# Kernel tuning notes

Measured on AMD Instinct MI355X. Metric: run time of the kernel, lower is better.

The kernel has to match this reference:

```python
import jax, jax.numpy as jnp
import numpy as np

H = 8          # num heads
LN_EPS = 1e-5  # torch LayerNorm default

_SHAPES = {
    'src': (1024, 8, 256), 'pos': (1024, 8, 256), 'query_embed': (80, 8, 256), 'cam_mask': (8, 80, 1024),
    'enc_qkv_w': (2, 768, 256), 'enc_qkv_b': (2, 768), 'enc_out_w': (2, 256, 256), 'enc_out_b': (2, 256),
    'enc_ln1_g': (2, 256), 'enc_ln1_b': (2, 256),
    'enc_ff1_w': (2, 2048, 256), 'enc_ff1_b': (2, 2048), 'enc_ff2_w': (2, 256, 2048), 'enc_ff2_b': (2, 256),
    'enc_ln2_g': (2, 256), 'enc_ln2_b': (2, 256),
    'dec_sa_qkv_w': (2, 768, 256), 'dec_sa_qkv_b': (2, 768), 'dec_sa_out_w': (2, 256, 256), 'dec_sa_out_b': (2, 256),
    'dec_ln1_g': (2, 256), 'dec_ln1_b': (2, 256),
    'dec_ca_qkv_w': (2, 768, 256), 'dec_ca_qkv_b': (2, 768), 'dec_ca_out_w': (2, 256, 256), 'dec_ca_out_b': (2, 256),
    'dec_ln2_g': (2, 256), 'dec_ln2_b': (2, 256),
    'dec_ff1_w': (2, 2048, 256), 'dec_ff1_b': (2, 2048), 'dec_ff2_w': (2, 256, 2048), 'dec_ff2_b': (2, 256),
    'dec_ln3_g': (2, 256), 'dec_ln3_b': (2, 256),
    'dec_norm_g': (256,), 'dec_norm_b': (256,),
}


def setup_inputs() -> dict:
    key = jax.random.key(0)
    out = {}
    for i, (name, sh) in enumerate(_SHAPES.items()):
        k = jax.random.fold_in(key, i)
        if name.endswith('_g'):
            out[name] = jnp.ones(sh, jnp.float32)
        elif name.endswith('ln1_b') or name.endswith('ln2_b') or name.endswith('ln3_b') or name == 'dec_norm_b':
            out[name] = jnp.zeros(sh, jnp.float32)
        else:
            scale = 1.0 if name in ('src', 'pos', 'query_embed', 'cam_mask') else 0.02
            out[name] = jax.random.normal(k, sh, dtype=jnp.float32) * scale
    return out


def layer_norm(x, g, b):
    mu = jnp.mean(x, axis=-1, keepdims=True)
    var = jnp.mean(jnp.square(x - mu), axis=-1, keepdims=True)
    return (x - mu) * jax.lax.rsqrt(var + LN_EPS) * g + b


def mha(q_in, k_in, v_in, qkv_w, qkv_b, out_w, out_b, bias=None):
    # q_in: [L,B,D], k_in/v_in: [S,B,D]; torch layout: projections are x @ W.T + b
    L, B, D = q_in.shape
    S = k_in.shape[0]
    hd = D // H
    wq, wk, wv = qkv_w[:D], qkv_w[D:2 * D], qkv_w[2 * D:]
    bq, bk, bv = qkv_b[:D], qkv_b[D:2 * D], qkv_b[2 * D:]
    q = (q_in @ wq.T + bq).reshape(L, B, H, hd).transpose(1, 2, 0, 3)  # [B,H,L,hd]
    k = (k_in @ wk.T + bk).reshape(S, B, H, hd).transpose(1, 2, 0, 3)  # [B,H,S,hd]
    v = (v_in @ wv.T + bv).reshape(S, B, H, hd).transpose(1, 2, 0, 3)
    logits = jnp.einsum('bhld,bhsd->bhls', q, k) * (1.0 / np.sqrt(hd))
    if bias is not None:
        logits = logits + bias[:, None, :, :]  # CAM bias broadcast over heads
    attn = jax.nn.softmax(logits, axis=-1)
    o = jnp.einsum('bhls,bhsd->bhld', attn, v).transpose(2, 0, 1, 3).reshape(L, B, D)
    return o @ out_w.T + out_b


def reference(src, pos, query_embed, cam_mask,
              enc_qkv_w, enc_qkv_b, enc_out_w, enc_out_b, enc_ln1_g, enc_ln1_b,
              enc_ff1_w, enc_ff1_b, enc_ff2_w, enc_ff2_b, enc_ln2_g, enc_ln2_b,
              dec_sa_qkv_w, dec_sa_qkv_b, dec_sa_out_w, dec_sa_out_b, dec_ln1_g, dec_ln1_b,
              dec_ca_qkv_w, dec_ca_qkv_b, dec_ca_out_w, dec_ca_out_b, dec_ln2_g, dec_ln2_b,
              dec_ff1_w, dec_ff1_b, dec_ff2_w, dec_ff2_b, dec_ln3_g, dec_ln3_b,
              dec_norm_g, dec_norm_b):
    n_enc = enc_qkv_w.shape[0]
    n_dec = dec_sa_qkv_w.shape[0]
    # --- encoder (post-norm DETR style, pos added to q,k) ---
    mem = src
    for i in range(n_enc):
        qk = mem + pos
        a = mha(qk, qk, mem, enc_qkv_w[i], enc_qkv_b[i], enc_out_w[i], enc_out_b[i])
        mem = layer_norm(mem + a, enc_ln1_g[i], enc_ln1_b[i])
        f = jax.nn.relu(mem @ enc_ff1_w[i].T + enc_ff1_b[i]) @ enc_ff2_w[i].T + enc_ff2_b[i]
        mem = layer_norm(mem + f, enc_ln2_g[i], enc_ln2_b[i])
    # --- decoder: tgt starts at zeros (Q2L), query_embed is query_pos ---
    tgt = jnp.zeros_like(query_embed)
    for i in range(n_dec):
        qk = tgt + query_embed
        sa = mha(qk, qk, tgt, dec_sa_qkv_w[i], dec_sa_qkv_b[i], dec_sa_out_w[i], dec_sa_out_b[i])
        tgt = layer_norm(tgt + sa, dec_ln1_g[i], dec_ln1_b[i])
        ca = mha(tgt + query_embed, mem + pos, mem,
                 dec_ca_qkv_w[i], dec_ca_qkv_b[i], dec_ca_out_w[i], dec_ca_out_b[i],
                 bias=cam_mask)  # MA: CAM-derived additive attention bias [B,L,S]
        tgt = layer_norm(tgt + ca, dec_ln2_g[i], dec_ln2_b[i])
        f = jax.nn.relu(tgt @ dec_ff1_w[i].T + dec_ff1_b[i]) @ dec_ff2_w[i].T + dec_ff2_b[i]
        tgt = layer_norm(tgt + f, dec_ln3_g[i], dec_ln3_b[i])
    out = layer_norm(tgt, dec_norm_g, dec_norm_b)
    return out[None]  # [1, L, B, D] as in TransformerDecoder's output.unsqueeze(0)
```

## Files before the change

### kernel.cpp

```cpp
#include <hip/hip_runtime.h>
#include <hip/hip_bf16.h>
#include <cstdint>
#include <cstddef>

typedef __hip_bfloat16 bf16;
typedef float f4 __attribute__((ext_vector_type(4)));
typedef float f32x4 __attribute__((ext_vector_type(4)));
typedef short s8v __attribute__((ext_vector_type(8)));
typedef unsigned short u16x4 __attribute__((ext_vector_type(4)));
typedef unsigned short u16x8 __attribute__((ext_vector_type(8)));

#define LN_EPS 1e-5f
#define LOG2E 1.4426950408889634f

#if __has_builtin(__builtin_amdgcn_exp2f)
__device__ __forceinline__ float EXP2(float x) { return __builtin_amdgcn_exp2f(x); }
#else
__device__ __forceinline__ float EXP2(float x) {
  float r; asm("v_exp_f32 %0, %1" : "=v"(r) : "v"(x)); return r;
}
#endif

__device__ __forceinline__ void async_cp16(const void* g, void* lds) {
  __builtin_amdgcn_global_load_lds(
      (const __attribute__((address_space(1))) unsigned int*)g,
      (__attribute__((address_space(3))) unsigned int*)lds, 16, 0, 0);
}

__device__ __forceinline__ uint32_t pkbf(float lo, float hi) {
#if __has_builtin(__builtin_amdgcn_perm)
  uint32_t l = __builtin_bit_cast(uint32_t, lo) + 0x8000u;
  uint32_t h = __builtin_bit_cast(uint32_t, hi) + 0x8000u;
  return __builtin_amdgcn_perm(h, l, 0x07060302u);
#else
  uint32_t l = __builtin_bit_cast(uint32_t, lo) + 0x8000u;
  uint32_t h = __builtin_bit_cast(uint32_t, hi) + 0x8000u;
  return (l >> 16) | (h & 0xFFFF0000u);
#endif
}

#define NCAST 16
struct CastArgs {
  const float* in[NCAST];
  bf16* out[NCAST];
  int end4[NCAST];
  int nseg;
};

__global__ __launch_bounds__(256) void cast_multi(CastArgs a, int total4) {
  int i = blockIdx.x * 256 + threadIdx.x;
  if (i >= total4) return;
  int s = 0;
  while (i >= a.end4[s]) ++s;
  int j = i - (s ? a.end4[s - 1] : 0);
  f4 v = ((const f4*)a.in[s])[j];
  u16x4 o;
#pragma unroll
  for (int c = 0; c < 4; ++c) {
    bf16 h = __float2bfloat16(v[c]);
    o[c] = *reinterpret_cast<unsigned short*>(&h);
  }
  ((u16x4*)a.out[s])[j] = o;
}

__global__ __launch_bounds__(256) void scale_f32_kernel(const float* __restrict__ in,
                                                        float* __restrict__ out,
                                                        float s, int n4) {
  int i = blockIdx.x * 256 + threadIdx.x;
  if (i < n4) {
    f4 v = ((const f4*)in)[i];
    ((f4*)out)[i] = v * s;
  }
}

__global__ __launch_bounds__(256) void add_bf16_kernel(const float* __restrict__ a,
                                                       const float* __restrict__ b,
                                                       bf16* __restrict__ out, int n4) {
  int i = blockIdx.x * 256 + threadIdx.x;
  if (i < n4) {
    f4 x = ((const f4*)a)[i];
    f4 y = ((const f4*)b)[i];
    u16x4 o;
#pragma unroll
    for (int j = 0; j < 4; ++j) {
      bf16 h = __float2bfloat16(x[j] + y[j]);
      o[j] = *reinterpret_cast<unsigned short*>(&h);
    }
    ((u16x4*)out)[i] = o;
  }
}

template <int TB, int MODE, int SPLITK>
__global__ __launch_bounds__(256, 2) void mfma_gemm(
    const bf16* __restrict__ A, const bf16* __restrict__ W,
    const float* __restrict__ bias, float* __restrict__ C,
    bf16* __restrict__ Cb, int M, int N, int K, int HL, float qscale) {
  constexpr int WM = TB / 2, WN = TB / 2;
  constexpr int MR = WM / 16, NR = WN / 16;
  constexpr int NCH = TB / 32;
  __shared__ __attribute__((aligned(16))) unsigned short SH[TB * 128];
  unsigned short (*As)[64] = (unsigned short(*)[64])SH;
  unsigned short (*Ws)[64] = (unsigned short(*)[64])(SH + TB * 64);
  const int tid = threadIdx.x;
  const int lane = tid & 63, wave = tid >> 6;
  const int wr = wave >> 1, wc = wave & 1;
  const int bm = blockIdx.x * TB, bn = blockIdx.y * TB;
  const int fr = lane & 15, fo = lane >> 4;
  const int srowi = lane >> 3;
  const int slot = lane & 7;
  const int gcol = (slot ^ srowi) * 8;

  const int kchunk = K / SPLITK;
  const int kbeg = (SPLITK > 1) ? blockIdx.z * kchunk : 0;

  f32x4 acc[MR][NR] = {};

  for (int k0 = kbeg; k0 < kbeg + kchunk; k0 += 64) {
    __syncthreads();
#pragma unroll
    for (int c = 0; c < NCH; ++c) {
      int rbase = wave * (TB / 4) + c * 8;
      int row = rbase + srowi;
      async_cp16(A + (size_t)(bm + row) * K + k0 + gcol, &As[rbase][0]);
      async_cp16(W + (size_t)(bn + row) * K + k0 + gcol, &Ws[rbase][0]);
    }
    __syncthreads();
#pragma unroll
    for (int ks = 0; ks < 2; ++ks) {
      s8v a[MR], b[NR];
#pragma unroll
      for (int mi = 0; mi < MR; ++mi) {
        int row = wr * WM + mi * 16 + fr;
        a[mi] = *(const s8v*)((const char*)&As[0][0] + row * 128 +
                              ((ks * 64 + fo * 16) ^ ((row & 7) << 4)));
      }
#pragma unroll
      for (int ni = 0; ni < NR; ++ni) {
        int row = wc * WN + ni * 16 + fr;
        b[ni] = *(const s8v*)((const char*)&Ws[0][0] + row * 128 +
                              ((ks * 64 + fo * 16) ^ ((row & 7) << 4)));
      }
#pragma unroll
      for (int mi = 0; mi < MR; ++mi)
#pragma unroll
        for (int ni = 0; ni < NR; ++ni)
          acc[mi][ni] = __builtin_amdgcn_mfma_f32_16x16x32_bf16(
              a[mi], b[ni], acc[mi][ni], 0, 0, 0);
    }
  }

  const int r0 = (lane >> 4) * 4;

  if (MODE == 5) {
    __syncthreads();
    unsigned short (*T)[72] = (unsigned short(*)[72])SH;
#pragma unroll
    for (int mi = 0; mi < MR; ++mi)
#pragma unroll
      for (int ni = 0; ni < NR; ++ni) {
        int colL = wc * WN + ni * 16 + fr;
        float bv = bias[bn + colL];
#pragma unroll
        for (int r = 0; r < 4; ++r) {
          int rowL = wr * WM + mi * 16 + r0 + r;
          bf16 hv = __float2bfloat16(acc[mi][ni][r] + bv);
          T[colL][rowL] = *(unsigned short*)&hv;
        }
      }
    __syncthreads();
    const int lbase = bm >> 3;
#pragma unroll
    for (int jj = 0; jj < 2; ++jj) {
      int cid = tid * 2 + jj;
      int colL = cid >> 3, bb = cid & 7;
      int c = bn + colL;
      int sec = c >> 8, hh = (c >> 5) & 7, d = c & 31;
      u16x8 v;
#pragma unroll
      for (int l = 0; l < 8; ++l) v[l] = T[colL][bb + 8 * l];
      *(u16x8*)(Cb + (size_t)sec * ((size_t)64 * 32 * HL) +
                ((size_t)(bb * 8 + hh) * 32 + d) * HL + lbase) = v;
    }
    return;
  }

  float* Cz = (MODE == 4) ? C + (size_t)blockIdx.z * M * N : C;
#pragma unroll
  for (int mi = 0; mi < MR; ++mi) {
#pragma unroll
    for (int ni = 0; ni < NR; ++ni) {
      int col = bn + wc * WN + ni * 16 + fr;
      float bv = (MODE == 4) ? 0.f : bias[col];
#pragma unroll
      for (int r = 0; r < 4; ++r) {
        int row = bm + wr * WM + mi * 16 + r0 + r;
        float t = acc[mi][ni][r] + bv;
        if (MODE == 2) t = fmaxf(t, 0.f);
        if (MODE == 0) {
          C[(size_t)row * N + col] = t;
        } else if (MODE == 4) {
          Cz[(size_t)row * N + col] = t;
        } else if (MODE == 3) {
          int l = row >> 3, bb = row & 7;
          int sec = col >> 8, hh = (col >> 5) & 7, d = col & 31;
          if (sec == 0) t *= qscale;
          Cb[(size_t)sec * ((size_t)64 * HL * 32) +
             ((size_t)(bb * 8 + hh) * HL + l) * 32 + d] = __float2bfloat16(t);
        } else {
          Cb[(size_t)row * N + col] = __float2bfloat16(t);
        }
      }
    }
  }
}

template <int HAS_BIAS, int PARTIAL, int NW>
__global__ __launch_bounds__(NW * 64, 3) void attn_mfma(
    const bf16* __restrict__ Qh, const bf16* __restrict__ Kh,
    const bf16* __restrict__ VhT, const float* __restrict__ bias,
    bf16* __restrict__ O, float* __restrict__ PO, float* __restrict__ PM,
    float* __restrict__ PL, int L, int S, int SC) {
  __shared__ __attribute__((aligned(16))) uint32_t Ps2[NW][2][16][36];
  const int tid = threadIdx.x;
  const int lane = tid & 63, wave = tid >> 6;
  const int fr = lane & 15, fo = lane >> 4;
  const int bh = blockIdx.x;
  const int b = bh >> 3, h = bh & 7;
  const int q0 = blockIdx.y * (NW * 16) + wave * 16;
  const int q = q0 + fr;

  const int cz = PARTIAL ? blockIdx.z : 0;
  const int sb = PARTIAL ? cz * SC : 0;
  const int se = PARTIAL ? min(S, sb + SC) : S;
  const int ng = (se - sb + 63) >> 6;

  s8v qf = {};
  if (q < L) qf = *(const s8v*)(Qh + ((size_t)bh * L + q) * 32 + fo * 8);

  const float* brow = nullptr;
  if (HAS_BIAS) brow = bias + ((size_t)b * L + (q < L ? q : L - 1)) * S;

  const bf16* Kbase = Kh + (size_t)bh * S * 32;
  const bf16* Vbase = VhT + (size_t)bh * 32 * S;

  float mA = -1e30f, lsA = 0.f, mB = -1e30f, lsB = 0.f;
  f32x4 oA[2] = {}, oB[2] = {};

  for (int g = 0; g < ng; g += 2) {
    const int sA = sb + g * 64, sB = sA + 64;

    s8v kA[4], kB[4], vA[2][2], vB[2][2];
#pragma unroll
    for (int kb = 0; kb < 4; ++kb) {
      kA[kb] = *(const s8v*)(Kbase + (size_t)(sA + kb * 16 + fr) * 32 + fo * 8);
      kB[kb] = *(const s8v*)(Kbase + (size_t)(sB + kb * 16 + fr) * 32 + fo * 8);
    }
#pragma unroll
    for (int dh = 0; dh < 2; ++dh)
#pragma unroll
      for (int ks = 0; ks < 2; ++ks) {
        vA[dh][ks] = *(const s8v*)(Vbase + (size_t)(dh * 16 + fr) * S +
                                   sA + ks * 32 + fo * 8);
        vB[dh][ks] = *(const s8v*)(Vbase + (size_t)(dh * 16 + fr) * S +
                                   sB + ks * 32 + fo * 8);
      }
    f4 bA[4], bB[4];
    if (HAS_BIAS) {
#pragma unroll
      for (int kb = 0; kb < 4; ++kb) {
        bA[kb] = *(const f4*)(brow + sA + kb * 16 + 4 * fo);
        bB[kb] = *(const f4*)(brow + sB + kb * 16 + 4 * fo);
      }
    }

    float lgA[16], lgB[16];
    __builtin_amdgcn_s_setprio(1);
#pragma unroll
    for (int kb = 0; kb < 4; ++kb) {
      f32x4 z = {};
      f32x4 sa = __builtin_amdgcn_mfma_f32_16x16x32_bf16(kA[kb], qf, z, 0, 0, 0);
#pragma unroll
      for (int r = 0; r < 4; ++r) lgA[kb * 4 + r] = sa[r];
    }
#pragma unroll
    for (int kb = 0; kb < 4; ++kb) {
      f32x4 z = {};
      f32x4 sa = __builtin_amdgcn_mfma_f32_16x16x32_bf16(kB[kb], qf, z, 0, 0, 0);
#pragma unroll
      for (int r = 0; r < 4; ++r) lgB[kb * 4 + r] = sa[r];
    }
    __builtin_amdgcn_s_setprio(0);
    if (HAS_BIAS) {
#pragma unroll
      for (int i = 0; i < 16; ++i) { lgA[i] += bA[i >> 2][i & 3]; lgB[i] += bB[i >> 2][i & 3]; }
    }
    if (sB + 64 > se) {
#pragma unroll
      for (int i = 0; i < 16; ++i) {
        int keyA = sA + (i >> 2) * 16 + 4 * fo + (i & 3);
        int keyB = sB + (i >> 2) * 16 + 4 * fo + (i & 3);
        if (keyA >= se) lgA[i] = -1e30f;
        if (keyB >= se) lgB[i] = -1e30f;
      }
    }

    float tA, tB;
    {
      float a0 = fmaxf(fmaxf(lgA[0], lgA[1]), fmaxf(lgA[2], lgA[3]));
      float a1 = fmaxf(fmaxf(lgA[4], lgA[5]), fmaxf(lgA[6], lgA[7]));
      float a2 = fmaxf(fmaxf(lgA[8], lgA[9]), fmaxf(lgA[10], lgA[11]));
      float a3 = fmaxf(fmaxf(lgA[12], lgA[13]), fmaxf(lgA[14], lgA[15]));
      tA = fmaxf(fmaxf(a0, a1), fmaxf(a2, a3));
      float b0 = fmaxf(fmaxf(lgB[0], lgB[1]), fmaxf(lgB[2], lgB[3]));
      float b1 = fmaxf(fmaxf(lgB[4], lgB[5]), fmaxf(lgB[6], lgB[7]));
      float b2 = fmaxf(fmaxf(lgB[8], lgB[9]), fmaxf(lgB[10], lgB[11]));
      float b3 = fmaxf(fmaxf(lgB[12], lgB[13]), fmaxf(lgB[14], lgB[15]));
      tB = fmaxf(fmaxf(b0, b1), fmaxf(b2, b3));
    }
    tA = fmaxf(tA, __shfl_xor(tA, 16));
    tB = fmaxf(tB, __shfl_xor(tB, 16));
    tA = fmaxf(tA, __shfl_xor(tA, 32));
    tB = fmaxf(tB, __shfl_xor(tB, 32));

    float nmA = fmaxf(mA, tA), nmB = fmaxf(mB, tB);
    float rsA = EXP2(mA - nmA), rsB = EXP2(mB - nmB);
    mA = nmA; mB = nmB;

    float psA = 0.f, psB = 0.f;
#pragma unroll
    for (int i = 0; i < 16; ++i) {
      lgA[i] = EXP2(lgA[i] - nmA); psA += lgA[i];
      lgB[i] = EXP2(lgB[i] - nmB); psB += lgB[i];
    }
    lsA = lsA * rsA + psA;
    lsB = lsB * rsB + psB;

#pragma unroll
    for (int kb = 0; kb < 4; ++kb) {
      uint32_t a0 = pkbf(lgA[kb * 4 + 0], lgA[kb * 4 + 1]);
      uint32_t a1 = pkbf(lgA[kb * 4 + 2], lgA[kb * 4 + 3]);
      *(uint64_t*)&Ps2[wave][0][fr][kb * 8 + 2 * fo] =
          (uint64_t)a0 | ((uint64_t)a1 << 32);
      uint32_t b0 = pkbf(lgB[kb * 4 + 0], lgB[kb * 4 + 1]);
      uint32_t b1 = pkbf(lgB[kb * 4 + 2], lgB[kb * 4 + 3]);
      *(uint64_t*)&Ps2[wave][1][fr][kb * 8 + 2 * fo] =
          (uint64_t)b0 | ((uint64_t)b1 << 32);
    }

#pragma unroll
    for (int r = 0; r < 4; ++r) {
      oA[0][r] *= rsA; oA[1][r] *= rsA;
      oB[0][r] *= rsB; oB[1][r] *= rsB;
    }
    s8v pA[2], pB[2];
#pragma unroll
    for (int ks = 0; ks < 2; ++ks) {
      pA[ks] = *(const s8v*)&Ps2[wave][0][fr][ks * 16 + 4 * fo];
      pB[ks] = *(const s8v*)&Ps2[wave][1][fr][ks * 16 + 4 * fo];
    }
    __builtin_amdgcn_s_setprio(1);
#pragma unroll
    for (int dh = 0; dh < 2; ++dh)
#pragma unroll
      for (int ks = 0; ks < 2; ++ks) {
        oA[dh] = __builtin_amdgcn_mfma_f32_16x16x32_bf16(vA[dh][ks], pA[ks], oA[dh], 0, 0, 0);
        oB[dh] = __builtin_amdgcn_mfma_f32_16x16x32_bf16(vB[dh][ks], pB[ks], oB[dh], 0, 0, 0);
      }
    __builtin_amdgcn_s_setprio(0);
  }

  float m = fmaxf(mA, mB);
  float wA = EXP2(mA - m), wB = EXP2(mB - m);
  float lsum = lsA * wA + lsB * wB;
  f32x4 oacc[2];
#pragma unroll
  for (int dh = 0; dh < 2; ++dh)
#pragma unroll
    for (int r = 0; r < 4; ++r)
      oacc[dh][r] = oA[dh][r] * wA + oB[dh][r] * wB;

  lsum += __shfl_xor(lsum, 16);
  lsum += __shfl_xor(lsum, 32);

  if (q < L) {
    if (PARTIAL) {
      size_t pi = ((size_t)cz * 64 + bh) * L + q;
      float* po = PO + pi * 32;
#pragma unroll
      for (int dh = 0; dh < 2; ++dh) {
        f4 t2;
#pragma unroll
        for (int r = 0; r < 4; ++r) t2[r] = oacc[dh][r];
        *(f4*)(po + dh * 16 + 4 * fo) = t2;
      }
      if (fo == 0) { PM[pi] = m; PL[pi] = lsum; }
    } else {
      float inv = 1.f / lsum;
      bf16* op = O + ((size_t)q * 8 + b) * 256 + h * 32;
#pragma unroll
      for (int dh = 0; dh < 2; ++dh) {
        uint32_t w0 = pkbf(oacc[dh][0] * inv, oacc[dh][1] * inv);
        uint32_t w1 = pkbf(oacc[dh][2] * inv, oacc[dh][3] * inv);
        *(uint32_t*)(op + dh * 16 + 4 * fo) = w0;
        *(uint32_t*)(op + dh * 16 + 4 * fo + 2) = w1;
      }
    }
  }
}

__global__ __launch_bounds__(256) void attn_combine(
    const float* __restrict__ PO, const float* __restrict__ PM,
    const float* __restrict__ PL, bf16* __restrict__ O, int L, int NC) {
  int gid = blockIdx.x * 256 + threadIdx.x;
  if (gid >= 64 * L * 32) return;
  int d = gid & 31;
  int rem = gid >> 5;
  int q = rem % L, bh = rem / L;
  int b = bh >> 3, h = bh & 7;
  float M = -1e30f;
  for (int c = 0; c < NC; ++c) M = fmaxf(M, PM[((size_t)c * 64 + bh) * L + q]);
  float lsum = 0.f, o = 0.f;
  for (int c = 0; c < NC; ++c) {
    size_t pi = ((size_t)c * 64 + bh) * L + q;
    float w = EXP2(PM[pi] - M);
    lsum += PL[pi] * w;
    o += PO[pi * 32 + d] * w;
  }
  O[((size_t)q * 8 + b) * 256 + h * 32 + d] = __float2bfloat16(o / lsum);
}

__global__ __launch_bounds__(256) void ln_kernel(
    const float* __restrict__ x, const float* __restrict__ res,
    const float* __restrict__ parts, int nparts, int pstride,
    const float* __restrict__ gbias,
    const float* __restrict__ g, const float* __restrict__ b,
    float* __restrict__ out, bf16* __restrict__ outb) {
  const int row = blockIdx.x, tid = threadIdx.x;
  size_t idx = (size_t)row * 256 + tid;
  float v = x[idx];
  if (res) v += res[idx];
  if (parts) {
    for (int z = 0; z < nparts; ++z) v += parts[(size_t)z * pstride + idx];
  }
  if (gbias) v += gbias[tid];
  float s = v, s2 = v * v;
#pragma unroll
  for (int off = 32; off >= 1; off >>= 1) {
    s += __shfl_down(s, off);
    s2 += __shfl_down(s2, off);
  }
  __shared__ float red[8];
  int wv = tid >> 6;
  if ((tid & 63) == 0) { red[wv] = s; red[4 + wv] = s2; }
  __syncthreads();
  if (tid == 0) {
    float ts = red[0] + red[1] + red[2] + red[3];
    float ts2 = red[4] + red[5] + red[6] + red[7];
    float mu = ts * (1.f / 256.f);
    float var = ts2 * (1.f / 256.f) - mu * mu;
    red[0] = mu;
    red[1] = rsqrtf(var + LN_EPS);
  }
  __syncthreads();
  float y = (v - red[0]) * red[1] * g[tid] + b[tid];
  if (out) out[idx] = y;
  if (outb) outb[idx] = __float2bfloat16(y);
}

extern "C" void kernel_launch(void* const* d_in, const int* in_sizes, int n_in,
                              void* d_out, int out_size, void* d_ws, size_t ws_size,
                              hipStream_t stream) {
  const float* src         = (const float*)d_in[0];
  const float* pos         = (const float*)d_in[1];
  const float* query_embed = (const float*)d_in[2];
  const float* cam_mask    = (const float*)d_in[3];
  const float* enc_qkv_w   = (const float*)d_in[4];
  const float* enc_qkv_b   = (const float*)d_in[5];
  const float* enc_out_w   = (const float*)d_in[6];
  const float* enc_out_b   = (const float*)d_in[7];
  const float* enc_ln1_g   = (const float*)d_in[8];
  const float* enc_ln1_b   = (const float*)d_in[9];
  const float* enc_ff1_w   = (const float*)d_in[10];
  const float* enc_ff1_b   = (const float*)d_in[11];
  const float* enc_ff2_w   = (const float*)d_in[12];
  const float* enc_ff2_b   = (const float*)d_in[13];
  const float* enc_ln2_g   = (const float*)d_in[14];
  const float* enc_ln2_b   = (const float*)d_in[15];
  const float* dec_sa_qkv_w= (const float*)d_in[16];
  const float* dec_sa_qkv_b= (const float*)d_in[17];
  const float* dec_sa_out_w= (const float*)d_in[18];
  const float* dec_sa_out_b= (const float*)d_in[19];
  const float* dec_ln1_g   = (const float*)d_in[20];
  const float* dec_ln1_b   = (const float*)d_in[21];
  const float* dec_ca_qkv_w= (const float*)d_in[22];
  const float* dec_ca_qkv_b= (const float*)d_in[23];
  const float* dec_ca_out_w= (const float*)d_in[24];
  const float* dec_ca_out_b= (const float*)d_in[25];
  const float* dec_ln2_g   = (const float*)d_in[26];
  const float* dec_ln2_b   = (const float*)d_in[27];
  const float* dec_ff1_w   = (const float*)d_in[28];
  const float* dec_ff1_b   = (const float*)d_in[29];
  const float* dec_ff2_w   = (const float*)d_in[30];
  const float* dec_ff2_b   = (const float*)d_in[31];
  const float* dec_ln3_g   = (const float*)d_in[32];
  const float* dec_ln3_b   = (const float*)d_in[33];
  const float* dec_norm_g  = (const float*)d_in[34];
  const float* dec_norm_b  = (const float*)d_in[35];

  size_t off = 0;
  char* base = (char*)d_ws;
  auto af = [&](size_t n) { float* p = (float*)(base + off); off += n * 4; return p; };
  auto ab = [&](size_t n) { bf16*  p = (bf16*)(base + off);  off += n * 2; return p; };

  float* mem  = af(2097152);
  float* r1   = af(2097152);
  float* PO   = af(8388608);
  float* pm   = af(262144);
  float* pl   = af(262144);
  float* cmlog= af(655360);
  float* pb   = af(1024);
  float* tgt  = af(163840);
  float* tpr  = af(163840);
  bf16* memb  = ab(2097152);
  bf16* qkb   = ab(2097152);
  bf16* aob   = ab(2097152);
  bf16* ffb   = ab(16777216);
  bf16* bufQ  = ab(4194304);
  bf16* bufK  = ab(4194304);
  bf16* bufV  = ab(4194304);
  bf16* bufVsa= ab(172032);
  bf16* tgtb  = ab(163840);
  bf16* tqkb  = ab(163840);
  bf16* taob  = ab(163840);
  bf16* tffb  = ab(1310720);
  bf16* w_enc_qkv = ab(393216);
  bf16* w_enc_out = ab(131072);
  bf16* w_enc_ff1 = ab(1048576);
  bf16* w_enc_ff2 = ab(1048576);
  bf16* w_sa_qkv  = ab(393216);
  bf16* w_sa_out  = ab(131072);
  bf16* w_ca_q    = ab(131072);
  bf16* w_ca_kv   = ab(262144);
  bf16* w_ca_out  = ab(131072);
  bf16* w_dec_ff1 = ab(1048576);
  bf16* w_dec_ff2 = ab(1048576);

  const float qscale = 0.17677669529663687f * LOG2E;

  {
    CastArgs ca;
    const float* ins[NCAST] = {
        enc_qkv_w, enc_out_w, enc_ff1_w, enc_ff2_w,
        dec_sa_qkv_w, dec_sa_out_w,
        dec_ca_qkv_w,
        dec_ca_qkv_w + 65536,
        dec_ca_qkv_w + 131072,
        dec_ca_qkv_w + 196608,
        dec_ca_qkv_w + 262144,
        dec_ca_qkv_w + 327680,
        dec_ca_out_w, dec_ff1_w, dec_ff2_w, src};
    bf16* outs[NCAST] = {
        w_enc_qkv, w_enc_out, w_enc_ff1, w_enc_ff2,
        w_sa_qkv, w_sa_out,
        w_ca_q,
        w_ca_kv,
        w_ca_kv + 131072,
        w_ca_q + 65536,
        w_ca_kv + 65536,
        w_ca_kv + 196608,
        w_ca_out, w_dec_ff1, w_dec_ff2, memb};
    int n4s[NCAST] = {98304, 32768, 262144, 262144, 98304, 32768,
                      16384, 16384, 16384, 16384, 16384, 16384,
                      32768, 262144, 262144, 524288};
    int acc = 0;
    for (int s = 0; s < NCAST; ++s) {
      ca.in[s] = ins[s]; ca.out[s] = outs[s];
      acc += n4s[s]; ca.end4[s] = acc;
    }
    ca.nseg = NCAST;
    cast_multi<<<(acc + 255) / 256, 256, 0, stream>>>(ca, acc);
  }
  scale_f32_kernel<<<640, 256, 0, stream>>>(cam_mask, cmlog, LOG2E, 163840);
  hipMemcpyAsync(mem, src, (size_t)2097152 * 4, hipMemcpyDeviceToDevice, stream);
  hipMemcpyAsync(pb,       dec_ca_qkv_b + 256,       1024, hipMemcpyDeviceToDevice, stream);
  hipMemcpyAsync(pb + 256, dec_ca_qkv_b + 768 + 256, 1024, hipMemcpyDeviceToDevice, stream);
  hipMemcpyAsync(pb + 512, dec_ca_qkv_b + 512,       1024, hipMemcpyDeviceToDevice, stream);
  hipMemcpyAsync(pb + 768, dec_ca_qkv_b + 768 + 512, 1024, hipMemcpyDeviceToDevice, stream);

  auto g64_f = [&](const bf16* A, const bf16* W, const float* bias, float* C,
                   int M, int N, int K) {
    mfma_gemm<64, 0, 1><<<dim3(M / 64, N / 64), 256, 0, stream>>>(
        A, W, bias, C, nullptr, M, N, K, 0, 1.f);
  };
  auto g64_head = [&](const bf16* A, const bf16* W, const float* bias, bf16* Cb,
                      int M, int N, int K, int HL, float qs) {
    mfma_gemm<64, 3, 1><<<dim3(M / 64, N / 64), 256, 0, stream>>>(
        A, W, bias, nullptr, Cb, M, N, K, HL, qs);
  };
  auto g64_headT = [&](const bf16* A, const bf16* W, const float* bias, bf16* Cb,
                       int M, int N, int K, int HL) {
    mfma_gemm<64, 5, 1><<<dim3(M / 64, N / 64), 256, 0, stream>>>(
        A, W, bias, nullptr, Cb, M, N, K, HL, 1.f);
  };
  auto g64_relu = [&](const bf16* A, const bf16* W, const float* bias, bf16* Cb,
                      int M, int N, int K) {
    mfma_gemm<64, 2, 1><<<dim3(M / 64, N / 64), 256, 0, stream>>>(
        A, W, bias, nullptr, Cb, M, N, K, 0, 1.f);
  };
  auto g128_relu = [&](const bf16* A, const bf16* W, const float* bias, bf16* Cb,
                       int M, int N, int K) {
    mfma_gemm<128, 2, 1><<<dim3(M / 128, N / 128), 256, 0, stream>>>(
        A, W, bias, nullptr, Cb, M, N, K, 0, 1.f);
  };

  for (int i = 0; i < 2; ++i) {
    const bf16* wq = w_enc_qkv + (size_t)i * 196608;
    const float* qkvb = enc_qkv_b + (size_t)i * 768;
    add_bf16_kernel<<<2048, 256, 0, stream>>>(mem, pos, qkb, 524288);
    g64_head(qkb, wq, qkvb, bufQ, 8192, 512, 256, 1024, qscale);
    g64_headT(memb, wq + 131072, qkvb + 512, bufV, 8192, 256, 256, 1024);
    attn_mfma<0, 0, 4><<<dim3(64, 16), 256, 0, stream>>>(
        bufQ, bufQ + 2097152, bufV, nullptr, aob, nullptr, nullptr, nullptr,
        1024, 1024, 0);
    g64_f(aob, w_enc_out + (size_t)i * 65536, enc_out_b + i * 256, r1,
          8192, 256, 256);
    ln_kernel<<<8192, 256, 0, stream>>>(mem, r1, nullptr, 0, 0, nullptr,
                                        enc_ln1_g + i * 256, enc_ln1_b + i * 256,
                                        mem, memb);
    g128_relu(memb, w_enc_ff1 + (size_t)i * 524288, enc_ff1_b + i * 2048, ffb,
              8192, 2048, 256);
    mfma_gemm<64, 4, 2><<<dim3(128, 4, 2), 256, 0, stream>>>(
        ffb, w_enc_ff2 + (size_t)i * 524288, nullptr, PO, nullptr,
        8192, 256, 2048, 0, 1.f);
    ln_kernel<<<8192, 256, 0, stream>>>(mem, nullptr, PO, 2, 2097152,
                                        enc_ff2_b + i * 256,
                                        enc_ln2_g + i * 256, enc_ln2_b + i * 256,
                                        mem, memb);
  }

  hipMemsetAsync(tgt, 0, (size_t)163840 * 4, stream);
  hipMemsetAsync(tgtb, 0, (size_t)163840 * 2, stream);
  add_bf16_kernel<<<2048, 256, 0, stream>>>(mem, pos, qkb, 524288);

  g64_head(qkb, w_ca_kv, pb, bufK, 8192, 512, 256, 1024, 1.f);
  g64_headT(memb, w_ca_kv + 131072, pb + 512, bufV, 8192, 512, 256, 1024);

  for (int i = 0; i < 2; ++i) {
    const bf16* wsa = w_sa_qkv + (size_t)i * 196608;
    const float* sab = dec_sa_qkv_b + (size_t)i * 768;
    const float* cab = dec_ca_qkv_b + (size_t)i * 768;

    add_bf16_kernel<<<160, 256, 0, stream>>>(tgt, query_embed, tqkb, 40960);
    g64_head(tqkb, wsa, sab, bufQ, 640, 512, 256, 80, qscale);
    g64_headT(tgtb, wsa + 131072, sab + 512, bufVsa, 640, 256, 256, 80);
    attn_mfma<0, 0, 1><<<dim3(64, 5), 64, 0, stream>>>(
        bufQ, bufQ + 163840, bufVsa, nullptr, taob, nullptr, nullptr, nullptr,
        80, 80, 0);
    g64_f(taob, w_sa_out + (size_t)i * 65536, dec_sa_out_b + i * 256, tpr,
          640, 256, 256);
    ln_kernel<<<640, 256, 0, stream>>>(tgt, tpr, nullptr, 0, 0, nullptr,
                                       dec_ln1_g + i * 256, dec_ln1_b + i * 256,
                                       tgt, tgtb);
    add_bf16_kernel<<<160, 256, 0, stream>>>(tgt, query_embed, tqkb, 40960);
    g64_head(tqkb, w_ca_q + (size_t)i * 65536, cab, bufQ, 640, 256, 256, 80, qscale);
    attn_mfma<1, 1, 1><<<dim3(64, 5, 8), 64, 0, stream>>>(
        bufQ, bufK + (size_t)i * 2097152, bufV + (size_t)i * 2097152, cmlog,
        nullptr, PO, pm, pl, 80, 1024, 128);
    attn_combine<<<640, 256, 0, stream>>>(PO, pm, pl, taob, 80, 8);
    g64_f(taob, w_ca_out + (size_t)i * 65536, dec_ca_out_b + i * 256, tpr,
          640, 256, 256);
    ln_kernel<<<640, 256, 0, stream>>>(tgt, tpr, nullptr, 0, 0, nullptr,
                                       dec_ln2_g + i * 256, dec_ln2_b + i * 256,
                                       tgt, tgtb);
    g64_relu(tgtb, w_dec_ff1 + (size_t)i * 524288, dec_ff1_b + i * 2048, tffb,
             640, 2048, 256);
    mfma_gemm<64, 4, 4><<<dim3(10, 4, 4), 256, 0, stream>>>(
        tffb, w_dec_ff2 + (size_t)i * 524288, nullptr, PO, nullptr,
        640, 256, 2048, 0, 1.f);
    ln_kernel<<<640, 256, 0, stream>>>(tgt, nullptr, PO, 4, 163840,
                                       dec_ff2_b + i * 256,
                                       dec_ln3_g + i * 256, dec_ln3_b + i * 256,
                                       tgt, tgtb);
  }

  ln_kernel<<<640, 256, 0, stream>>>(tgt, nullptr, nullptr, 0, 0, nullptr,
                                     dec_norm_g, dec_norm_b,
                                     (float*)d_out, nullptr);
}
```

Before: 433.0 us.

## Fuse positional adds into LayerNorm and split-K out-projections into LN partial sums

LayerNorm gains an auxiliary output that writes bf16(y + aux), so the separate add kernels for mem+pos and tgt+query_embed are dropped. query_embed is cast once for the first decoder self-attention, where tgt is zero. The attention out-projections now use split-K GEMMs that write partial sums, and LayerNorm reduces those partials plus the bias, replacing the old single-pass GEMM and residual buffer. This removes several small launches and intermediate round trips, but adds extra partial-buffer traffic and redistributes GEMM work into split-K blocks.

```diff
diff --git a/kernel.cpp b/kernel.cpp
--- a/kernel.cpp
+++ b/kernel.cpp
@@ -39,7 +39,7 @@
 #endif
 }
 
-#define NCAST 16
+#define NCAST 17
 struct CastArgs {
   const float* in[NCAST];
   bf16* out[NCAST];
@@ -434,7 +434,8 @@
     const float* __restrict__ parts, int nparts, int pstride,
     const float* __restrict__ gbias,
     const float* __restrict__ g, const float* __restrict__ b,
-    float* __restrict__ out, bf16* __restrict__ outb) {
+    float* __restrict__ out, bf16* __restrict__ outb,
+    const float* __restrict__ aux, bf16* __restrict__ auxb) {
   const int row = blockIdx.x, tid = threadIdx.x;
   size_t idx = (size_t)row * 256 + tid;
   float v = x[idx];
@@ -465,6 +466,7 @@
   float y = (v - red[0]) * red[1] * g[tid] + b[tid];
   if (out) out[idx] = y;
   if (outb) outb[idx] = __float2bfloat16(y);
+  if (auxb) auxb[idx] = __float2bfloat16(y + aux[idx]);
 }
 
 extern "C" void kernel_launch(void* const* d_in, const int* in_sizes, int n_in,
@@ -520,7 +522,6 @@
   float* cmlog= af(655360);
   float* pb   = af(1024);
   float* tgt  = af(163840);
-  float* tpr  = af(163840);
   bf16* memb  = ab(2097152);
   bf16* qkb   = ab(2097152);
   bf16* aob   = ab(2097152);
@@ -532,6 +533,7 @@
   bf16* tgtb  = ab(163840);
   bf16* tqkb  = ab(163840);
   bf16* taob  = ab(163840);
+  bf16* qeb   = ab(163840);
   bf16* tffb  = ab(1310720);
   bf16* w_enc_qkv = ab(393216);
   bf16* w_enc_out = ab(131072);
@@ -558,7 +560,7 @@
         dec_ca_qkv_w + 196608,
         dec_ca_qkv_w + 262144,
         dec_ca_qkv_w + 327680,
-        dec_ca_out_w, dec_ff1_w, dec_ff2_w, src};
+        dec_ca_out_w, dec_ff1_w, dec_ff2_w, src, query_embed};
     bf16* outs[NCAST] = {
         w_enc_qkv, w_enc_out, w_enc_ff1, w_enc_ff2,
         w_sa_qkv, w_sa_out,
@@ -568,10 +570,10 @@
         w_ca_q + 65536,
         w_ca_kv + 65536,
         w_ca_kv + 196608,
-        w_ca_out, w_dec_ff1, w_dec_ff2, memb};
+        w_ca_out, w_dec_ff1, w_dec_ff2, memb, qeb};
     int n4s[NCAST] = {98304, 32768, 262144, 262144, 98304, 32768,
                       16384, 16384, 16384, 16384, 16384, 16384,
-                      32768, 262144, 262144, 524288};
+                      32768, 262144, 262144, 524288, 40960};
     int acc = 0;
     for (int s = 0; s < NCAST; ++s) {
       ca.in[s] = ins[s]; ca.out[s] = outs[s];
@@ -587,11 +589,6 @@
   hipMemcpyAsync(pb + 512, dec_ca_qkv_b + 512,       1024, hipMemcpyDeviceToDevice, stream);
   hipMemcpyAsync(pb + 768, dec_ca_qkv_b + 768 + 512, 1024, hipMemcpyDeviceToDevice, stream);
 
-  auto g64_f = [&](const bf16* A, const bf16* W, const float* bias, float* C,
-                   int M, int N, int K) {
-    mfma_gemm<64, 0, 1><<<dim3(M / 64, N / 64), 256, 0, stream>>>(
-        A, W, bias, C, nullptr, M, N, K, 0, 1.f);
-  };
   auto g64_head = [&](const bf16* A, const bf16* W, const float* bias, bf16* Cb,
                       int M, int N, int K, int HL, float qs) {
     mfma_gemm<64, 3, 1><<<dim3(M / 64, N / 64), 256, 0, stream>>>(
@@ -613,20 +610,22 @@
         A, W, bias, nullptr, Cb, M, N, K, 0, 1.f);
   };
 
+  add_bf16_kernel<<<2048, 256, 0, stream>>>(mem, pos, qkb, 524288);
   for (int i = 0; i < 2; ++i) {
     const bf16* wq = w_enc_qkv + (size_t)i * 196608;
     const float* qkvb = enc_qkv_b + (size_t)i * 768;
-    add_bf16_kernel<<<2048, 256, 0, stream>>>(mem, pos, qkb, 524288);
     g64_head(qkb, wq, qkvb, bufQ, 8192, 512, 256, 1024, qscale);
     g64_headT(memb, wq + 131072, qkvb + 512, bufV, 8192, 256, 256, 1024);
     attn_mfma<0, 0, 4><<<dim3(64, 16), 256, 0, stream>>>(
         bufQ, bufQ + 2097152, bufV, nullptr, aob, nullptr, nullptr, nullptr,
         1024, 1024, 0);
-    g64_f(aob, w_enc_out + (size_t)i * 65536, enc_out_b + i * 256, r1,
-          8192, 256, 256);
-    ln_kernel<<<8192, 256, 0, stream>>>(mem, r1, nullptr, 0, 0, nullptr,
+    mfma_gemm<64, 4, 2><<<dim3(128, 4, 2), 256, 0, stream>>>(
+        aob, w_enc_out + (size_t)i * 65536, nullptr, PO, nullptr,
+        8192, 256, 256, 0, 1.f);
+    ln_kernel<<<8192, 256, 0, stream>>>(mem, nullptr, PO, 2, 2097152,
+                                        enc_out_b + i * 256,
                                         enc_ln1_g + i * 256, enc_ln1_b + i * 256,
-                                        mem, memb);
+                                        mem, memb, nullptr, nullptr);
     g128_relu(memb, w_enc_ff1 + (size_t)i * 524288, enc_ff1_b + i * 2048, ffb,
               8192, 2048, 256);
     mfma_gemm<64, 4, 2><<<dim3(128, 4, 2), 256, 0, stream>>>(
@@ -635,12 +634,11 @@
     ln_kernel<<<8192, 256, 0, stream>>>(mem, nullptr, PO, 2, 2097152,
                                         enc_ff2_b + i * 256,
                                         enc_ln2_g + i * 256, enc_ln2_b + i * 256,
-                                        mem, memb);
+                                        mem, memb, pos, qkb);
   }
 
   hipMemsetAsync(tgt, 0, (size_t)163840 * 4, stream);
   hipMemsetAsync(tgtb, 0, (size_t)163840 * 2, stream);
-  add_bf16_kernel<<<2048, 256, 0, stream>>>(mem, pos, qkb, 524288);
 
   g64_head(qkb, w_ca_kv, pb, bufK, 8192, 512, 256, 1024, 1.f);
   g64_headT(memb, w_ca_kv + 131072, pb + 512, bufV, 8192, 512, 256, 1024);
@@ -649,29 +647,32 @@
     const bf16* wsa = w_sa_qkv + (size_t)i * 196608;
     const float* sab = dec_sa_qkv_b + (size_t)i * 768;
     const float* cab = dec_ca_qkv_b + (size_t)i * 768;
-
-    add_bf16_kernel<<<160, 256, 0, stream>>>(tgt, query_embed, tqkb, 40960);
-    g64_head(tqkb, wsa, sab, bufQ, 640, 512, 256, 80, qscale);
+    const bf16* sa_in = (i == 0) ? qeb : tqkb;
+
+    g64_head(sa_in, wsa, sab, bufQ, 640, 512, 256, 80, qscale);
     g64_headT(tgtb, wsa + 131072, sab + 512, bufVsa, 640, 256, 256, 80);
     attn_mfma<0, 0, 1><<<dim3(64, 5), 64, 0, stream>>>(
         bufQ, bufQ + 163840, bufVsa, nullptr, taob, nullptr, nullptr, nullptr,
         80, 80, 0);
-    g64_f(taob, w_sa_out + (size_t)i * 65536, dec_sa_out_b + i * 256, tpr,
-          640, 256, 256);
-    ln_kernel<<<640, 256, 0, stream>>>(tgt, tpr, nullptr, 0, 0, nullptr,
+    mfma_gemm<64, 4, 4><<<dim3(10, 4, 4), 256, 0, stream>>>(
+        taob, w_sa_out + (size_t)i * 65536, nullptr, PO, nullptr,
+        640, 256, 256, 0, 1.f);
+    ln_kernel<<<640, 256, 0, stream>>>(tgt, nullptr, PO, 4, 163840,
+                                       dec_sa_out_b + i * 256,
                                        dec_ln1_g + i * 256, dec_ln1_b + i * 256,
-                                       tgt, tgtb);
-    add_bf16_kernel<<<160, 256, 0, stream>>>(tgt, query_embed, tqkb, 40960);
+                                       tgt, tgtb, query_embed, tqkb);
     g64_head(tqkb, w_ca_q + (size_t)i * 65536, cab, bufQ, 640, 256, 256, 80, qscale);
     attn_mfma<1, 1, 1><<<dim3(64, 5, 8), 64, 0, stream>>>(
         bufQ, bufK + (size_t)i * 2097152, bufV + (size_t)i * 2097152, cmlog,
-        nullptr, PO, pm, pl, 80, 1024, 128);
-    attn_combine<<<640, 256, 0, stream>>>(PO, pm, pl, taob, 80, 8);
-    g64_f(taob, w_ca_out + (size_t)i * 65536, dec_ca_out_b + i * 256, tpr,
-          640, 256, 256);
-    ln_kernel<<<640, 256, 0, stream>>>(tgt, tpr, nullptr, 0, 0, nullptr,
+        nullptr, PO + 4194304, pm, pl, 80, 1024, 128);
+    attn_combine<<<640, 256, 0, stream>>>(PO + 4194304, pm, pl, taob, 80, 8);
+    mfma_gemm<64, 4, 4><<<dim3(10, 4, 4), 256, 0, stream>>>(
+        taob, w_ca_out + (size_t)i * 65536, nullptr, PO, nullptr,
+        640, 256, 256, 0, 1.f);
+    ln_kernel<<<640, 256, 0, stream>>>(tgt, nullptr, PO, 4, 163840,
+                                       dec_ca_out_b + i * 256,
                                        dec_ln2_g + i * 256, dec_ln2_b + i * 256,
-                                       tgt, tgtb);
+                                       tgt, tgtb, nullptr, nullptr);
     g64_relu(tgtb, w_dec_ff1 + (size_t)i * 524288, dec_ff1_b + i * 2048, tffb,
              640, 2048, 256);
     mfma_gemm<64, 4, 4><<<dim3(10, 4, 4), 256, 0, stream>>>(
@@ -680,10 +681,10 @@
     ln_kernel<<<640, 256, 0, stream>>>(tgt, nullptr, PO, 4, 163840,
                                        dec_ff2_b + i * 256,
                                        dec_ln3_g + i * 256, dec_ln3_b + i * 256,
-                                       tgt, tgtb);
+                                       tgt, tgtb, query_embed, tqkb);
   }
 
   ln_kernel<<<640, 256, 0, stream>>>(tgt, nullptr, nullptr, 0, 0, nullptr,
                                      dec_norm_g, dec_norm_b,
-                                     (float*)d_out, nullptr);
-}
+                                     (float*)d_out, nullptr, nullptr, nullptr);
+}
```

Measured after the change: 422.6 us. 1.02x faster.
